# Kernel optimization log

Hardware: AMD Instinct MI355X
Metric: run time of the kernel (lower is better)

## Reference

```python
import jax, jax.numpy as jnp
import numpy as np

NUM_NETS = 100_000
PINS_PER_NET = 5
NUM_PINS = NUM_NETS * PINS_PER_NET
XL, XH, YL, YH = 0.0, 1000.0, 0.0, 1000.0
NUM_BINS_X = 512
NUM_BINS_Y = 512
BIN_SIZE_X = (XH - XL) / NUM_BINS_X
BIN_SIZE_Y = (YH - YL) / NUM_BINS_Y
NUM_H_TRACKS = 100.0
NUM_V_TRACKS = 100.0
MAX_RATE = 2.0
MIN_RATE = 1.0 / MAX_RATE


def setup_inputs() -> dict:
    key = jax.random.key(0)
    k1, k2, k3 = jax.random.split(key, 3)
    px = jax.random.uniform(k1, (NUM_PINS,), jnp.float32, XL, XH)
    py = jax.random.uniform(k2, (NUM_PINS,), jnp.float32, YL, YH)
    pin_pos = jnp.concatenate([px, py])  # [2*num_pins]: x then y
    netpin_start = (jnp.arange(NUM_NETS + 1, dtype=jnp.int32) * PINS_PER_NET)
    flat_netpin = jax.random.permutation(k3, NUM_PINS).astype(jnp.int32)
    net_weights = jnp.ones((NUM_NETS,), jnp.float32)
    return {"pin_pos": pin_pos, "netpin_start": netpin_start,
            "flat_netpin": flat_netpin, "net_weights": net_weights}


def reference(pin_pos, netpin_start, flat_netpin, net_weights):
    num_pins = flat_netpin.shape[0]
    # segment id of each flat pin slot (which net it belongs to)
    seg = jnp.searchsorted(netpin_start, jnp.arange(num_pins, dtype=netpin_start.dtype), side="right") - 1
    x = pin_pos[flat_netpin]                     # [num_pins]
    y = pin_pos[num_pins + flat_netpin]          # [num_pins]
    # per-net bounding boxes
    x_min = jax.ops.segment_min(x, seg, num_segments=NUM_NETS)
    x_max = jax.ops.segment_max(x, seg, num_segments=NUM_NETS)
    y_min = jax.ops.segment_min(y, seg, num_segments=NUM_NETS)
    y_max = jax.ops.segment_max(y, seg, num_segments=NUM_NETS)
    # fractional overlap of each net bbox with each bin column/row
    ex = XL + BIN_SIZE_X * jnp.arange(NUM_BINS_X + 1, dtype=pin_pos.dtype)
    ey = YL + BIN_SIZE_Y * jnp.arange(NUM_BINS_Y + 1, dtype=pin_pos.dtype)
    ox = jnp.maximum(jnp.minimum(x_max[:, None], ex[None, 1:]) -
                     jnp.maximum(x_min[:, None], ex[None, :-1]), 0.0)  # [N, Bx]
    oy = jnp.maximum(jnp.minimum(y_max[:, None], ey[None, 1:]) -
                     jnp.maximum(y_min[:, None], ey[None, :-1]), 0.0)  # [N, By]
    # RUDY: horizontal density wt/(y_max-y_min), vertical density wt/(x_max-x_min)
    wh = net_weights / (y_max - y_min)
    wv = net_weights / (x_max - x_min)
    h_map = jnp.einsum("nx,ny->xy", ox * wh[:, None], oy)
    v_map = jnp.einsum("nx,ny->xy", ox * wv[:, None], oy)
    h_map = h_map * (1.0 / (BIN_SIZE_X * NUM_H_TRACKS))
    v_map = v_map * (1.0 / (BIN_SIZE_Y * NUM_V_TRACKS))
    route = jnp.maximum(jnp.abs(h_map), jnp.abs(v_map))
    return jnp.clip(route * route, MIN_RATE, MAX_RATE)
```

## Files before the change

### kernel.cpp

```cpp
#include <hip/hip_runtime.h>

#define NUM_NETS     100000
#define PINS_PER_NET 5
#define NUM_PINS     (NUM_NETS * PINS_PER_NET)
#define NB           512
#define BIN_H        1.953125f
#define INV_H        0.512f
#define OUT_SCALE    (1.0f / 195.3125f)

#define SW           8
#define NSTRIPES     (NB / SW)
#define CAP          24576

#define FXS          2097152.0f
#define INV_FXS      (1.0f / 2097152.0f)

__global__ void zero_kernel(int* __restrict__ gcur) {
    gcur[threadIdx.x] = 0;
}

__global__ __launch_bounds__(256) void bbox_emit_kernel(
        const float* __restrict__ pin_pos,
        const int*   __restrict__ flat_netpin,
        const float* __restrict__ net_weights,
        int* __restrict__ gcur,
        float4* __restrict__ bucket) {
    __shared__ int lcnt[NSTRIPES];
    __shared__ int lbase[NSTRIPES];
    int tid = threadIdx.x;
    if (tid < NSTRIPES) lcnt[tid] = 0;
    __syncthreads();

    int n = blockIdx.x * 256 + tid;
    bool valid = n < NUM_NETS;
    float xmn = 1e30f, xmx = -1e30f, ymn = 1e30f, ymx = -1e30f;
    float wh = 0.f, wv = 0.f;
    int kx1 = 0, kx2 = 0;
    if (valid) {
#pragma unroll
        for (int p = 0; p < PINS_PER_NET; ++p) {
            int pi  = flat_netpin[n * PINS_PER_NET + p];
            float x = pin_pos[pi];
            float y = pin_pos[NUM_PINS + pi];
            xmn = fminf(xmn, x); xmx = fmaxf(xmx, x);
            ymn = fminf(ymn, y); ymx = fmaxf(ymx, y);
        }
        float w = net_weights[n];
        wh = w / (ymx - ymn);
        wv = w / (xmx - xmn);
        kx1 = min(NB - 1, (int)(xmn * INV_H));
        kx2 = min(NB - 1, (int)(xmx * INV_H));
#pragma unroll
        for (int cx = 0; cx < 2; ++cx) {
            int kx = cx ? kx2 : kx1;
            int s0 = kx >> 3;
            atomicAdd(&lcnt[s0], 2);
            if (kx + 1 < NB && ((kx + 1) >> 3) != s0)
                atomicAdd(&lcnt[(kx + 1) >> 3], 2);
        }
    }
    __syncthreads();
    if (tid < NSTRIPES) {
        lbase[tid] = atomicAdd(&gcur[tid], lcnt[tid]);
        lcnt[tid] = 0;
    }
    __syncthreads();
    if (valid) {
#pragma unroll
        for (int cx = 0; cx < 2; ++cx) {
            int   kx = cx ? kx2 : kx1;
            float xc = cx ? xmx : xmn;
            int s0 = kx >> 3;
            int s1 = (kx + 1 < NB) ? ((kx + 1) >> 3) : s0;
#pragma unroll
            for (int cy = 0; cy < 2; ++cy) {
                float yc = cy ? ymx : ymn;
                float sg = ((cx ^ cy) ? -1.0f : 1.0f);
                float4 item = make_float4(xc, yc, sg * wh, sg * wv);
                {
                    int rank = atomicAdd(&lcnt[s0], 1);
                    int pos  = lbase[s0] + rank;
                    if (pos < CAP) bucket[(size_t)s0 * CAP + pos] = item;
                }
                if (s1 != s0) {
                    int rank = atomicAdd(&lcnt[s1], 1);
                    int pos  = lbase[s1] + rank;
                    if (pos < CAP) bucket[(size_t)s1 * CAP + pos] = item;
                }
            }
        }
    }
}

__global__ __launch_bounds__(1024) void stripe_finish_kernel(
        const float4* __restrict__ bucket,
        const int* __restrict__ gcur,
        float* __restrict__ Th,  float* __restrict__ Tv,
        int* __restrict__ flag,
        float* __restrict__ out) {
    __shared__ int   acc[2 * SW * NB];
    __shared__ float wsc[32];
    __shared__ float offHs[2][NB];
    __shared__ float offVs[2][NB];
    int st  = blockIdx.x;
    int tid = threadIdx.x;
    int x0  = st * SW;
    int* accH = acc;
    int* accV = acc + SW * NB;
    float* fH = (float*)accH;
    float* fV = (float*)accV;

    for (int k = tid; k < 2 * SW * NB; k += 1024) acc[k] = 0;
    __syncthreads();

    int cnt = min(gcur[st], CAP);
    const float4* bk = bucket + (size_t)st * CAP;
    for (int q = tid; q < cnt; q += 1024) {
        float4 it = bk[q];
        int kx = min(NB - 1, (int)(it.x * INV_H));
        int ky = min(NB - 1, (int)(it.y * INV_H));
        float dx0 = (kx + 1) * BIN_H - it.x;
        float dx1 = it.x - kx * BIN_H;
        float dy0 = (ky + 1) * BIN_H - it.y;
        float dy1 = it.y - ky * BIN_H;
        bool y1ok = (ky + 1) < NB;
        int c = kx - x0;
#pragma unroll
        for (int cc = 0; cc < 2; ++cc) {
            int col = c + cc;
            if ((unsigned)col < SW) {
                float dx = cc ? dx1 : dx0;
                int b = col * NB + ky;
                atomicAdd(&accH[b], __float2int_rn(it.z * dx * dy0 * FXS));
                atomicAdd(&accV[b], __float2int_rn(it.w * dx * dy0 * FXS));
                if (y1ok) {
                    atomicAdd(&accH[b + 1], __float2int_rn(it.z * dx * dy1 * FXS));
                    atomicAdd(&accV[b + 1], __float2int_rn(it.w * dx * dy1 * FXS));
                }
            }
        }
    }
    __syncthreads();

    int half = tid >> 9;
    int y    = tid & 511;
    int lane = tid & 63;
    int wv16 = tid >> 6;
    int wrow0 = half * 8;
#pragma unroll
    for (int rp = 0; rp < 4; ++rp) {
        int row = rp * 2 + half;
        float vH = (float)accH[row * NB + y] * INV_FXS;
        float vV = (float)accV[row * NB + y] * INV_FXS;
#pragma unroll
        for (int o = 1; o < 64; o <<= 1) {
            float a = __shfl_up(vH, o);
            float b = __shfl_up(vV, o);
            if (lane >= o) { vH += a; vV += b; }
        }
        if (lane == 63) { wsc[wv16] = vH; wsc[16 + wv16] = vV; }
        __syncthreads();
        float oh = 0.f, ov = 0.f;
        for (int j = wrow0; j < wv16; ++j) { oh += wsc[j]; ov += wsc[16 + j]; }
        fH[row * NB + y] = vH + oh;
        fV[row * NB + y] = vV + ov;
        __syncthreads();
    }

    if (tid < NB) {
        float f = 0.f;
#pragma unroll
        for (int rr = 0; rr < SW; ++rr) {
            int i = rr * NB + tid;
            f += fH[i]; fH[i] = f;
        }
        __hip_atomic_store(&Th[st * NB + tid], f, __ATOMIC_RELAXED,
                           __HIP_MEMORY_SCOPE_AGENT);
    } else {
        int yy = tid - NB;
        float f = 0.f;
#pragma unroll
        for (int rr = 0; rr < SW; ++rr) {
            int i = rr * NB + yy;
            f += fV[i]; fV[i] = f;
        }
        __hip_atomic_store(&Tv[st * NB + yy], f, __ATOMIC_RELAXED,
                           __HIP_MEMORY_SCOPE_AGENT);
    }
    __syncthreads();
    if (tid == 0) {
        __threadfence();
        __hip_atomic_store(&flag[st], 1, __ATOMIC_RELEASE,
                           __HIP_MEMORY_SCOPE_AGENT);
    }

    if (tid < st) {
        while (__hip_atomic_load(&flag[tid], __ATOMIC_ACQUIRE,
                                 __HIP_MEMORY_SCOPE_AGENT) == 0) { }
    }
    __syncthreads();
    {
        float sh = 0.f, sv = 0.f;
        for (int s2 = half; s2 < st; s2 += 2) {
            sh += __hip_atomic_load(&Th[s2 * NB + y], __ATOMIC_RELAXED,
                                    __HIP_MEMORY_SCOPE_AGENT);
            sv += __hip_atomic_load(&Tv[s2 * NB + y], __ATOMIC_RELAXED,
                                    __HIP_MEMORY_SCOPE_AGENT);
        }
        offHs[half][y] = sh;
        offVs[half][y] = sv;
    }
    __syncthreads();

    {
        float offh = offHs[0][y] + offHs[1][y];
        float offv = offVs[0][y] + offVs[1][y];
#pragma unroll
        for (int r2 = 0; r2 < 4; ++r2) {
            int rr = half * 4 + r2;
            float h = fabsf(fH[rr * NB + y] + offh) * OUT_SCALE;
            float v = fabsf(fV[rr * NB + y] + offv) * OUT_SCALE;
            float m = fmaxf(h, v);
            out[(x0 + rr) * NB + y] = fminf(fmaxf(m * m, 0.5f), 2.0f);
        }
    }
}

__global__ void scatter_kernel(const float* __restrict__ pin_pos,
                               const int*   __restrict__ flat_netpin,
                               const float* __restrict__ net_weights,
                               float* __restrict__ Uh,
                               float* __restrict__ Uv) {
    int n = blockIdx.x * blockDim.x + threadIdx.x;
    if (n >= NUM_NETS) return;
    float xmn = 1e30f, xmx = -1e30f, ymn = 1e30f, ymx = -1e30f;
#pragma unroll
    for (int p = 0; p < PINS_PER_NET; ++p) {
        int pi  = flat_netpin[n * PINS_PER_NET + p];
        float x = pin_pos[pi];
        float y = pin_pos[NUM_PINS + pi];
        xmn = fminf(xmn, x); xmx = fmaxf(xmx, x);
        ymn = fminf(ymn, y); ymx = fmaxf(ymx, y);
    }
    float w  = net_weights[n];
    float wh = w / (ymx - ymn), wv = w / (xmx - xmn);
    int kx1 = min(NB - 1, (int)(xmn * INV_H));
    int kx2 = min(NB - 1, (int)(xmx * INV_H));
    int ky1 = min(NB - 1, (int)(ymn * INV_H));
    int ky2 = min(NB - 1, (int)(ymx * INV_H));
    int   xi[4] = { kx1, kx1 + 1, kx2, kx2 + 1 };
    float xv[4] = { (kx1 + 1) * BIN_H - xmn,  xmn - kx1 * BIN_H,
                    xmx - (kx2 + 1) * BIN_H,  kx2 * BIN_H - xmx };
    int   yi[4] = { ky1, ky1 + 1, ky2, ky2 + 1 };
    float yv[4] = { (ky1 + 1) * BIN_H - ymn,  ymn - ky1 * BIN_H,
                    ymx - (ky2 + 1) * BIN_H,  ky2 * BIN_H - ymx };
#pragma unroll
    for (int a = 0; a < 4; ++a) {
        if (xi[a] >= NB) continue;
#pragma unroll
        for (int b2 = 0; b2 < 4; ++b2) {
            if (yi[b2] >= NB) continue;
            float prod = xv[a] * yv[b2];
            atomicAdd(&Uh[xi[a] * NB + yi[b2]], wh * prod);
            atomicAdd(&Uv[xi[a] * NB + yi[b2]], wv * prod);
        }
    }
}

__global__ void fb_rowscan_kernel(float* __restrict__ Uh, float* __restrict__ Uv) {
    __shared__ float sh[NB];
    __shared__ float sv[NB];
    int rr = blockIdx.x, t = threadIdx.x;
    sh[t] = Uh[rr * NB + t];
    sv[t] = Uv[rr * NB + t];
    __syncthreads();
#pragma unroll
    for (int off = 1; off < NB; off <<= 1) {
        float a = (t >= off) ? sh[t - off] : 0.0f;
        float b = (t >= off) ? sv[t - off] : 0.0f;
        __syncthreads();
        sh[t] += a; sv[t] += b;
        __syncthreads();
    }
    Uh[rr * NB + t] = sh[t];
    Uv[rr * NB + t] = sv[t];
}

__global__ void fb_colscan_kernel(const float* __restrict__ Uh,
                                  const float* __restrict__ Uv,
                                  float* __restrict__ out) {
    int t = blockIdx.x * blockDim.x + threadIdx.x;
    if (t >= NB) return;
    float sh = 0.f, sv = 0.f;
    for (int i = 0; i < NB; ++i) {
        sh += Uh[i * NB + t];
        sv += Uv[i * NB + t];
        float h = fabsf(sh) * OUT_SCALE;
        float v = fabsf(sv) * OUT_SCALE;
        float m = fmaxf(h, v);
        out[i * NB + t] = fminf(fmaxf(m * m, 0.5f), 2.0f);
    }
}

extern "C" void kernel_launch(void* const* d_in, const int* in_sizes, int n_in,
                              void* d_out, int out_size, void* d_ws, size_t ws_size,
                              hipStream_t stream) {
    const float* pin_pos     = (const float*)d_in[0];
    const int*   flat_netpin = (const int*)d_in[2];
    const float* net_weights = (const float*)d_in[3];
    float* out = (float*)d_out;
    float* ws  = (float*)d_ws;

    const size_t o_cur = 0;
    const size_t o_flg = 64;
    const size_t o_bkt = 128;
    const size_t o_Th  = o_bkt + (size_t)NSTRIPES * CAP * 4;
    const size_t o_Tv  = o_Th + (size_t)NSTRIPES * NB;
    const size_t need  = o_Tv + (size_t)NSTRIPES * NB;

    if (ws_size < need * sizeof(float)) {
        float* Uh = ws;
        float* Uv = ws + (size_t)NB * NB;
        hipMemsetAsync(ws, 0, 2 * (size_t)NB * NB * sizeof(float), stream);
        scatter_kernel<<<(NUM_NETS + 255) / 256, 256, 0, stream>>>(
            pin_pos, flat_netpin, net_weights, Uh, Uv);
        fb_rowscan_kernel<<<NB, NB, 0, stream>>>(Uh, Uv);
        fb_colscan_kernel<<<2, 256, 0, stream>>>(Uh, Uv, out);
        return;
    }

    int*    gcur   = (int*)(ws + o_cur);
    int*    flg    = (int*)(ws + o_flg);
    float4* bucket = (float4*)(ws + o_bkt);
    float*  Th     = ws + o_Th;
    float*  Tv     = ws + o_Tv;

    zero_kernel<<<1, 128, 0, stream>>>(gcur);

    bbox_emit_kernel<<<(NUM_NETS + 255) / 256, 256, 0, stream>>>(
        pin_pos, flat_netpin, net_weights, gcur, bucket);

    stripe_finish_kernel<<<NSTRIPES, 1024, 0, stream>>>(
        bucket, gcur, Th, Tv, flg, out);
}
```

Baseline: 50.56 us.

## Fuse bbox emission and stripe finish into one persistent kernel with grid barrier

Merges the bounding-box/bucket-emit kernel and the per-stripe accumulation kernel into a single launch of 256 blocks of 1024 threads. The two phases are separated by a device-wide atomic counter barrier, and the 64 stripe blocks then continue on their own. Bucket items become pairs of relaxed 64-bit atomic stores and loads so they are visible across blocks without a kernel boundary. The global stripe-counter atomic is skipped when a block has nothing for that stripe. This removes a kernel launch gap, but all 256 blocks must be co-resident or the barrier deadlocks. Each thread now handles nets at block granularity 1024, which leaves many blocks idle in the emit phase.

```diff
diff --git a/kernel.cpp b/kernel.cpp
--- a/kernel.cpp
+++ b/kernel.cpp
@@ -11,27 +11,37 @@
 #define SW           8
 #define NSTRIPES     (NB / SW)
 #define CAP          24576
+#define GBLK         256
 
 #define FXS          2097152.0f
 #define INV_FXS      (1.0f / 2097152.0f)
 
-__global__ void zero_kernel(int* __restrict__ gcur) {
-    gcur[threadIdx.x] = 0;
-}
-
-__global__ __launch_bounds__(256) void bbox_emit_kernel(
+__global__ void zero_kernel(int* __restrict__ p) {
+    if (threadIdx.x < 160) p[threadIdx.x] = 0;
+}
+
+__global__ __launch_bounds__(1024) void fused_kernel(
         const float* __restrict__ pin_pos,
         const int*   __restrict__ flat_netpin,
         const float* __restrict__ net_weights,
         int* __restrict__ gcur,
-        float4* __restrict__ bucket) {
-    __shared__ int lcnt[NSTRIPES];
-    __shared__ int lbase[NSTRIPES];
+        unsigned long long* __restrict__ bkt64,
+        float* __restrict__ Th,  float* __restrict__ Tv,
+        int* __restrict__ flag, int* __restrict__ done,
+        float* __restrict__ out) {
+    __shared__ int   lcnt[NSTRIPES];
+    __shared__ int   lbase[NSTRIPES];
+    __shared__ int   acc[2 * SW * NB];
+    __shared__ float wsc[32];
+    __shared__ float offHs[2][NB];
+    __shared__ float offVs[2][NB];
     int tid = threadIdx.x;
+    int bid = blockIdx.x;
+
     if (tid < NSTRIPES) lcnt[tid] = 0;
     __syncthreads();
 
-    int n = blockIdx.x * 256 + tid;
+    int n = bid * 1024 + tid;
     bool valid = n < NUM_NETS;
     float xmn = 1e30f, xmx = -1e30f, ymn = 1e30f, ymx = -1e30f;
     float wh = 0.f, wv = 0.f;
@@ -61,7 +71,8 @@
     }
     __syncthreads();
     if (tid < NSTRIPES) {
-        lbase[tid] = atomicAdd(&gcur[tid], lcnt[tid]);
+        int c = lcnt[tid];
+        lbase[tid] = c ? atomicAdd(&gcur[tid], c) : 0;
         lcnt[tid] = 0;
     }
     __syncthreads();
@@ -76,35 +87,52 @@
             for (int cy = 0; cy < 2; ++cy) {
                 float yc = cy ? ymx : ymn;
                 float sg = ((cx ^ cy) ? -1.0f : 1.0f);
-                float4 item = make_float4(xc, yc, sg * wh, sg * wv);
+                unsigned long long lo =
+                    (unsigned long long)__float_as_uint(xc) |
+                    ((unsigned long long)__float_as_uint(yc) << 32);
+                unsigned long long hi =
+                    (unsigned long long)__float_as_uint(sg * wh) |
+                    ((unsigned long long)__float_as_uint(sg * wv) << 32);
                 {
                     int rank = atomicAdd(&lcnt[s0], 1);
                     int pos  = lbase[s0] + rank;
-                    if (pos < CAP) bucket[(size_t)s0 * CAP + pos] = item;
+                    if (pos < CAP) {
+                        size_t ip = ((size_t)s0 * CAP + pos) * 2;
+                        __hip_atomic_store(&bkt64[ip], lo, __ATOMIC_RELAXED,
+                                           __HIP_MEMORY_SCOPE_AGENT);
+                        __hip_atomic_store(&bkt64[ip + 1], hi, __ATOMIC_RELAXED,
+                                           __HIP_MEMORY_SCOPE_AGENT);
+                    }
                 }
                 if (s1 != s0) {
                     int rank = atomicAdd(&lcnt[s1], 1);
                     int pos  = lbase[s1] + rank;
-                    if (pos < CAP) bucket[(size_t)s1 * CAP + pos] = item;
+                    if (pos < CAP) {
+                        size_t ip = ((size_t)s1 * CAP + pos) * 2;
+                        __hip_atomic_store(&bkt64[ip], lo, __ATOMIC_RELAXED,
+                                           __HIP_MEMORY_SCOPE_AGENT);
+                        __hip_atomic_store(&bkt64[ip + 1], hi, __ATOMIC_RELAXED,
+                                           __HIP_MEMORY_SCOPE_AGENT);
+                    }
                 }
             }
         }
     }
-}
-
-__global__ __launch_bounds__(1024) void stripe_finish_kernel(
-        const float4* __restrict__ bucket,
-        const int* __restrict__ gcur,
-        float* __restrict__ Th,  float* __restrict__ Tv,
-        int* __restrict__ flag,
-        float* __restrict__ out) {
-    __shared__ int   acc[2 * SW * NB];
-    __shared__ float wsc[32];
-    __shared__ float offHs[2][NB];
-    __shared__ float offVs[2][NB];
-    int st  = blockIdx.x;
-    int tid = threadIdx.x;
-    int x0  = st * SW;
+    __syncthreads();
+
+    if (tid == 0) {
+        atomicAdd(done, 1);
+        while (__hip_atomic_load(done, __ATOMIC_ACQUIRE,
+                                 __HIP_MEMORY_SCOPE_AGENT) < GBLK) {
+            __builtin_amdgcn_s_sleep(4);
+        }
+    }
+    __syncthreads();
+
+    if (bid >= NSTRIPES) return;
+
+    int st = bid;
+    int x0 = st * SW;
     int* accH = acc;
     int* accV = acc + SW * NB;
     float* fH = (float*)accH;
@@ -113,16 +141,24 @@
     for (int k = tid; k < 2 * SW * NB; k += 1024) acc[k] = 0;
     __syncthreads();
 
-    int cnt = min(gcur[st], CAP);
-    const float4* bk = bucket + (size_t)st * CAP;
+    int cnt = min(__hip_atomic_load(&gcur[st], __ATOMIC_RELAXED,
+                                    __HIP_MEMORY_SCOPE_AGENT), CAP);
     for (int q = tid; q < cnt; q += 1024) {
-        float4 it = bk[q];
-        int kx = min(NB - 1, (int)(it.x * INV_H));
-        int ky = min(NB - 1, (int)(it.y * INV_H));
-        float dx0 = (kx + 1) * BIN_H - it.x;
-        float dx1 = it.x - kx * BIN_H;
-        float dy0 = (ky + 1) * BIN_H - it.y;
-        float dy1 = it.y - ky * BIN_H;
+        size_t ip = ((size_t)st * CAP + q) * 2;
+        unsigned long long lo = __hip_atomic_load(&bkt64[ip], __ATOMIC_RELAXED,
+                                                  __HIP_MEMORY_SCOPE_AGENT);
+        unsigned long long hi = __hip_atomic_load(&bkt64[ip + 1], __ATOMIC_RELAXED,
+                                                  __HIP_MEMORY_SCOPE_AGENT);
+        float ix = __uint_as_float((unsigned)lo);
+        float iy = __uint_as_float((unsigned)(lo >> 32));
+        float iz = __uint_as_float((unsigned)hi);
+        float iw = __uint_as_float((unsigned)(hi >> 32));
+        int kx = min(NB - 1, (int)(ix * INV_H));
+        int ky = min(NB - 1, (int)(iy * INV_H));
+        float dx0 = (kx + 1) * BIN_H - ix;
+        float dx1 = ix - kx * BIN_H;
+        float dy0 = (ky + 1) * BIN_H - iy;
+        float dy1 = iy - ky * BIN_H;
         bool y1ok = (ky + 1) < NB;
         int c = kx - x0;
 #pragma unroll
@@ -131,11 +167,11 @@
             if ((unsigned)col < SW) {
                 float dx = cc ? dx1 : dx0;
                 int b = col * NB + ky;
-                atomicAdd(&accH[b], __float2int_rn(it.z * dx * dy0 * FXS));
-                atomicAdd(&accV[b], __float2int_rn(it.w * dx * dy0 * FXS));
+                atomicAdd(&accH[b], __float2int_rn(iz * dx * dy0 * FXS));
+                atomicAdd(&accV[b], __float2int_rn(iw * dx * dy0 * FXS));
                 if (y1ok) {
-                    atomicAdd(&accH[b + 1], __float2int_rn(it.z * dx * dy1 * FXS));
-                    atomicAdd(&accV[b + 1], __float2int_rn(it.w * dx * dy1 * FXS));
+                    atomicAdd(&accH[b + 1], __float2int_rn(iz * dx * dy1 * FXS));
+                    atomicAdd(&accV[b + 1], __float2int_rn(iw * dx * dy1 * FXS));
                 }
             }
         }
@@ -196,7 +232,9 @@
 
     if (tid < st) {
         while (__hip_atomic_load(&flag[tid], __ATOMIC_ACQUIRE,
-                                 __HIP_MEMORY_SCOPE_AGENT) == 0) { }
+                                 __HIP_MEMORY_SCOPE_AGENT) == 0) {
+            __builtin_amdgcn_s_sleep(2);
+        }
     }
     __syncthreads();
     {
@@ -311,12 +349,13 @@
     float* out = (float*)d_out;
     float* ws  = (float*)d_ws;
 
-    const size_t o_cur = 0;
-    const size_t o_flg = 64;
-    const size_t o_bkt = 128;
-    const size_t o_Th  = o_bkt + (size_t)NSTRIPES * CAP * 4;
-    const size_t o_Tv  = o_Th + (size_t)NSTRIPES * NB;
-    const size_t need  = o_Tv + (size_t)NSTRIPES * NB;
+    const size_t o_cur  = 0;
+    const size_t o_flg  = 64;
+    const size_t o_done = 128;
+    const size_t o_bkt  = 160;
+    const size_t o_Th   = o_bkt + (size_t)NSTRIPES * CAP * 4;
+    const size_t o_Tv   = o_Th + (size_t)NSTRIPES * NB;
+    const size_t need   = o_Tv + (size_t)NSTRIPES * NB;
 
     if (ws_size < need * sizeof(float)) {
         float* Uh = ws;
@@ -329,17 +368,15 @@
         return;
     }
 
-    int*    gcur   = (int*)(ws + o_cur);
-    int*    flg    = (int*)(ws + o_flg);
-    float4* bucket = (float4*)(ws + o_bkt);
-    float*  Th     = ws + o_Th;
-    float*  Tv     = ws + o_Tv;
-
-    zero_kernel<<<1, 128, 0, stream>>>(gcur);
-
-    bbox_emit_kernel<<<(NUM_NETS + 255) / 256, 256, 0, stream>>>(
-        pin_pos, flat_netpin, net_weights, gcur, bucket);
-
-    stripe_finish_kernel<<<NSTRIPES, 1024, 0, stream>>>(
-        bucket, gcur, Th, Tv, flg, out);
-}
+    int*                gcur  = (int*)(ws + o_cur);
+    int*                flg   = (int*)(ws + o_flg);
+    int*                done  = (int*)(ws + o_done);
+    unsigned long long* bkt64 = (unsigned long long*)(ws + o_bkt);
+    float*              Th    = ws + o_Th;
+    float*              Tv    = ws + o_Tv;
+
+    zero_kernel<<<1, 256, 0, stream>>>((int*)ws);
+
+    fused_kernel<<<GBLK, 1024, 0, stream>>>(
+        pin_pos, flat_netpin, net_weights, gcur, bkt64, Th, Tv, flg, done, out);
+}
```

Result: slower. 157.6 us (+211.7%).

## Split each x-stripe into two y-half blocks with cross-block row-total exchange

Applied to the files above, without the earlier changes.

Buckets are now keyed by stripe and y-half, so the finish stage launches twice as many blocks, each owning an 8x256 tile instead of 8x512. Items whose cell straddles the y=255/256 boundary are emitted to both halves. The upper-half block waits on a flag for the lower half's per-row totals to complete its y prefix scan, and the cross-stripe lookback now runs per half. The aim is more CU parallelism and less shared-memory atomic and scan work per block. The cost is extra emitted items, an additional inter-block spin dependency, and reliance on all blocks being co-resident.

```diff
diff --git a/kernel.cpp b/kernel.cpp
--- a/kernel.cpp
+++ b/kernel.cpp
@@ -10,13 +10,15 @@
 
 #define SW           8
 #define NSTRIPES     (NB / SW)
-#define CAP          24576
+#define NBK          (NSTRIPES * 2)
+#define HH           256
+#define CAP          12288
 
 #define FXS          2097152.0f
 #define INV_FXS      (1.0f / 2097152.0f)
 
-__global__ void zero_kernel(int* __restrict__ gcur) {
-    gcur[threadIdx.x] = 0;
+__global__ void zero_kernel(int* __restrict__ p) {
+    if (threadIdx.x < 320) p[threadIdx.x] = 0;
 }
 
 __global__ __launch_bounds__(256) void bbox_emit_kernel(
@@ -25,17 +27,17 @@
         const float* __restrict__ net_weights,
         int* __restrict__ gcur,
         float4* __restrict__ bucket) {
-    __shared__ int lcnt[NSTRIPES];
-    __shared__ int lbase[NSTRIPES];
+    __shared__ int lcnt[NBK];
+    __shared__ int lbase[NBK];
     int tid = threadIdx.x;
-    if (tid < NSTRIPES) lcnt[tid] = 0;
+    if (tid < NBK) lcnt[tid] = 0;
     __syncthreads();
 
     int n = blockIdx.x * 256 + tid;
     bool valid = n < NUM_NETS;
     float xmn = 1e30f, xmx = -1e30f, ymn = 1e30f, ymx = -1e30f;
     float wh = 0.f, wv = 0.f;
-    int kx1 = 0, kx2 = 0;
+    int kx1 = 0, kx2 = 0, ky1 = 0, ky2 = 0;
     if (valid) {
 #pragma unroll
         for (int p = 0; p < PINS_PER_NET; ++p) {
@@ -50,18 +52,31 @@
         wv = w / (xmx - xmn);
         kx1 = min(NB - 1, (int)(xmn * INV_H));
         kx2 = min(NB - 1, (int)(xmx * INV_H));
+        ky1 = min(NB - 1, (int)(ymn * INV_H));
+        ky2 = min(NB - 1, (int)(ymx * INV_H));
 #pragma unroll
         for (int cx = 0; cx < 2; ++cx) {
             int kx = cx ? kx2 : kx1;
             int s0 = kx >> 3;
-            atomicAdd(&lcnt[s0], 2);
-            if (kx + 1 < NB && ((kx + 1) >> 3) != s0)
-                atomicAdd(&lcnt[(kx + 1) >> 3], 2);
-        }
-    }
-    __syncthreads();
-    if (tid < NSTRIPES) {
-        lbase[tid] = atomicAdd(&gcur[tid], lcnt[tid]);
+            int s1 = (kx + 1 < NB && ((kx + 1) >> 3) != s0) ? ((kx + 1) >> 3) : -1;
+#pragma unroll
+            for (int cy = 0; cy < 2; ++cy) {
+                int ky = cy ? ky2 : ky1;
+                int hh = ky >> 8;
+                bool ystr = (ky == 255);
+                atomicAdd(&lcnt[(s0 << 1) | hh], 1);
+                if (ystr)     atomicAdd(&lcnt[(s0 << 1) | 1], 1);
+                if (s1 >= 0) {
+                    atomicAdd(&lcnt[(s1 << 1) | hh], 1);
+                    if (ystr) atomicAdd(&lcnt[(s1 << 1) | 1], 1);
+                }
+            }
+        }
+    }
+    __syncthreads();
+    if (tid < NBK) {
+        int c = lcnt[tid];
+        lbase[tid] = c ? atomicAdd(&gcur[tid], c) : 0;
         lcnt[tid] = 0;
     }
     __syncthreads();
@@ -71,157 +86,211 @@
             int   kx = cx ? kx2 : kx1;
             float xc = cx ? xmx : xmn;
             int s0 = kx >> 3;
-            int s1 = (kx + 1 < NB) ? ((kx + 1) >> 3) : s0;
+            int s1 = (kx + 1 < NB && ((kx + 1) >> 3) != s0) ? ((kx + 1) >> 3) : -1;
 #pragma unroll
             for (int cy = 0; cy < 2; ++cy) {
+                int   ky = cy ? ky2 : ky1;
                 float yc = cy ? ymx : ymn;
+                int hh = ky >> 8;
+                bool ystr = (ky == 255);
                 float sg = ((cx ^ cy) ? -1.0f : 1.0f);
                 float4 item = make_float4(xc, yc, sg * wh, sg * wv);
-                {
-                    int rank = atomicAdd(&lcnt[s0], 1);
-                    int pos  = lbase[s0] + rank;
-                    if (pos < CAP) bucket[(size_t)s0 * CAP + pos] = item;
+                int bs[4]; int nb = 0;
+                bs[nb++] = (s0 << 1) | hh;
+                if (ystr)     bs[nb++] = (s0 << 1) | 1;
+                if (s1 >= 0) {
+                    bs[nb++] = (s1 << 1) | hh;
+                    if (ystr) bs[nb++] = (s1 << 1) | 1;
                 }
-                if (s1 != s0) {
-                    int rank = atomicAdd(&lcnt[s1], 1);
-                    int pos  = lbase[s1] + rank;
-                    if (pos < CAP) bucket[(size_t)s1 * CAP + pos] = item;
+                for (int j = 0; j < nb; ++j) {
+                    int b = bs[j];
+                    int rank = atomicAdd(&lcnt[b], 1);
+                    int pos  = lbase[b] + rank;
+                    if (pos < CAP) bucket[(size_t)b * CAP + pos] = item;
                 }
             }
         }
     }
 }
 
-__global__ __launch_bounds__(1024) void stripe_finish_kernel(
+__global__ __launch_bounds__(1024) void half_stripe_kernel(
         const float4* __restrict__ bucket,
         const int* __restrict__ gcur,
+        float* __restrict__ rtH, float* __restrict__ rtV,
+        int* __restrict__ flagRT,
         float* __restrict__ Th,  float* __restrict__ Tv,
-        int* __restrict__ flag,
+        int* __restrict__ flagT,
         float* __restrict__ out) {
-    __shared__ int   acc[2 * SW * NB];
-    __shared__ float wsc[32];
-    __shared__ float offHs[2][NB];
-    __shared__ float offVs[2][NB];
-    int st  = blockIdx.x;
+    __shared__ int   acc[2 * SW * HH];
+    __shared__ float wsc[4][4][2];
+    __shared__ float rowtH[8], rowtV[8];
+    __shared__ float btH[8],  btV[8];
+    __shared__ float offH[4][HH];
+    __shared__ float offV[4][HH];
+    int bid = blockIdx.x;
+    int st  = bid >> 1;
+    int h   = bid & 1;
     int tid = threadIdx.x;
     int x0  = st * SW;
+    int y0  = h * HH;
     int* accH = acc;
-    int* accV = acc + SW * NB;
+    int* accV = acc + SW * HH;
     float* fH = (float*)accH;
     float* fV = (float*)accV;
 
-    for (int k = tid; k < 2 * SW * NB; k += 1024) acc[k] = 0;
-    __syncthreads();
-
-    int cnt = min(gcur[st], CAP);
-    const float4* bk = bucket + (size_t)st * CAP;
+    for (int k = tid; k < 2 * SW * HH; k += 1024) acc[k] = 0;
+    __syncthreads();
+
+    int cnt = min(gcur[bid], CAP);
+    const float4* bk = bucket + (size_t)bid * CAP;
     for (int q = tid; q < cnt; q += 1024) {
         float4 it = bk[q];
         int kx = min(NB - 1, (int)(it.x * INV_H));
         int ky = min(NB - 1, (int)(it.y * INV_H));
+        int gy = ky - y0;
         float dx0 = (kx + 1) * BIN_H - it.x;
         float dx1 = it.x - kx * BIN_H;
         float dy0 = (ky + 1) * BIN_H - it.y;
         float dy1 = it.y - ky * BIN_H;
-        bool y1ok = (ky + 1) < NB;
+        bool ok0 = (unsigned)gy < (unsigned)HH;
+        bool ok1 = (ky + 1 < NB) && ((unsigned)(gy + 1) < (unsigned)HH);
         int c = kx - x0;
 #pragma unroll
         for (int cc = 0; cc < 2; ++cc) {
             int col = c + cc;
             if ((unsigned)col < SW) {
                 float dx = cc ? dx1 : dx0;
-                int b = col * NB + ky;
-                atomicAdd(&accH[b], __float2int_rn(it.z * dx * dy0 * FXS));
-                atomicAdd(&accV[b], __float2int_rn(it.w * dx * dy0 * FXS));
-                if (y1ok) {
-                    atomicAdd(&accH[b + 1], __float2int_rn(it.z * dx * dy1 * FXS));
-                    atomicAdd(&accV[b + 1], __float2int_rn(it.w * dx * dy1 * FXS));
+                if (ok0) {
+                    int b = col * HH + gy;
+                    atomicAdd(&accH[b], __float2int_rn(it.z * dx * dy0 * FXS));
+                    atomicAdd(&accV[b], __float2int_rn(it.w * dx * dy0 * FXS));
+                }
+                if (ok1) {
+                    int b = col * HH + gy + 1;
+                    atomicAdd(&accH[b], __float2int_rn(it.z * dx * dy1 * FXS));
+                    atomicAdd(&accV[b], __float2int_rn(it.w * dx * dy1 * FXS));
                 }
             }
         }
     }
     __syncthreads();
 
-    int half = tid >> 9;
-    int y    = tid & 511;
     int lane = tid & 63;
-    int wv16 = tid >> 6;
-    int wrow0 = half * 8;
-#pragma unroll
-    for (int rp = 0; rp < 4; ++rp) {
-        int row = rp * 2 + half;
-        float vH = (float)accH[row * NB + y] * INV_FXS;
-        float vV = (float)accV[row * NB + y] * INV_FXS;
+    int wwi  = (tid >> 6) & 3;
+    int rg   = tid >> 8;
+    int y    = tid & 255;
+#pragma unroll
+    for (int pass = 0; pass < 2; ++pass) {
+        int row = pass * 4 + rg;
+        float vH = (float)accH[row * HH + y] * INV_FXS;
+        float vV = (float)accV[row * HH + y] * INV_FXS;
 #pragma unroll
         for (int o = 1; o < 64; o <<= 1) {
             float a = __shfl_up(vH, o);
             float b = __shfl_up(vV, o);
             if (lane >= o) { vH += a; vV += b; }
         }
-        if (lane == 63) { wsc[wv16] = vH; wsc[16 + wv16] = vV; }
+        if (lane == 63) { wsc[rg][wwi][0] = vH; wsc[rg][wwi][1] = vV; }
         __syncthreads();
         float oh = 0.f, ov = 0.f;
-        for (int j = wrow0; j < wv16; ++j) { oh += wsc[j]; ov += wsc[16 + j]; }
-        fH[row * NB + y] = vH + oh;
-        fV[row * NB + y] = vV + ov;
-        __syncthreads();
-    }
-
-    if (tid < NB) {
+        for (int j = 0; j < wwi; ++j) { oh += wsc[rg][j][0]; ov += wsc[rg][j][1]; }
+        vH += oh; vV += ov;
+        fH[row * HH + y] = vH;
+        fV[row * HH + y] = vV;
+        if (lane == 63 && wwi == 3) { rowtH[row] = vH; rowtV[row] = vV; }
+        __syncthreads();
+    }
+
+    if (h == 0) {
+        if (tid < 8) {
+            __hip_atomic_store(&rtH[st * 8 + tid], rowtH[tid], __ATOMIC_RELAXED,
+                               __HIP_MEMORY_SCOPE_AGENT);
+            __hip_atomic_store(&rtV[st * 8 + tid], rowtV[tid], __ATOMIC_RELAXED,
+                               __HIP_MEMORY_SCOPE_AGENT);
+        }
+        if (tid < 8) { btH[tid] = 0.f; btV[tid] = 0.f; }
+        __syncthreads();
+        if (tid == 0) {
+            __threadfence();
+            __hip_atomic_store(&flagRT[st], 1, __ATOMIC_RELEASE,
+                               __HIP_MEMORY_SCOPE_AGENT);
+        }
+    } else {
+        if (tid == 0) {
+            while (__hip_atomic_load(&flagRT[st], __ATOMIC_ACQUIRE,
+                                     __HIP_MEMORY_SCOPE_AGENT) == 0) {
+                __builtin_amdgcn_s_sleep(2);
+            }
+        }
+        __syncthreads();
+        if (tid < 8) {
+            btH[tid] = __hip_atomic_load(&rtH[st * 8 + tid], __ATOMIC_RELAXED,
+                                         __HIP_MEMORY_SCOPE_AGENT);
+            btV[tid] = __hip_atomic_load(&rtV[st * 8 + tid], __ATOMIC_RELAXED,
+                                         __HIP_MEMORY_SCOPE_AGENT);
+        }
+        __syncthreads();
+    }
+
+    if (tid < HH) {
         float f = 0.f;
 #pragma unroll
         for (int rr = 0; rr < SW; ++rr) {
-            int i = rr * NB + tid;
-            f += fH[i]; fH[i] = f;
-        }
-        __hip_atomic_store(&Th[st * NB + tid], f, __ATOMIC_RELAXED,
+            int i = rr * HH + tid;
+            f += fH[i] + btH[rr];
+            fH[i] = f;
+        }
+        __hip_atomic_store(&Th[bid * HH + tid], f, __ATOMIC_RELAXED,
                            __HIP_MEMORY_SCOPE_AGENT);
-    } else {
-        int yy = tid - NB;
+    } else if (tid < 2 * HH) {
+        int yy = tid - HH;
         float f = 0.f;
 #pragma unroll
         for (int rr = 0; rr < SW; ++rr) {
-            int i = rr * NB + yy;
-            f += fV[i]; fV[i] = f;
-        }
-        __hip_atomic_store(&Tv[st * NB + yy], f, __ATOMIC_RELAXED,
+            int i = rr * HH + yy;
+            f += fV[i] + btV[rr];
+            fV[i] = f;
+        }
+        __hip_atomic_store(&Tv[bid * HH + yy], f, __ATOMIC_RELAXED,
                            __HIP_MEMORY_SCOPE_AGENT);
     }
     __syncthreads();
     if (tid == 0) {
         __threadfence();
-        __hip_atomic_store(&flag[st], 1, __ATOMIC_RELEASE,
+        __hip_atomic_store(&flagT[bid], 1, __ATOMIC_RELEASE,
                            __HIP_MEMORY_SCOPE_AGENT);
     }
 
     if (tid < st) {
-        while (__hip_atomic_load(&flag[tid], __ATOMIC_ACQUIRE,
-                                 __HIP_MEMORY_SCOPE_AGENT) == 0) { }
+        while (__hip_atomic_load(&flagT[tid * 2 + h], __ATOMIC_ACQUIRE,
+                                 __HIP_MEMORY_SCOPE_AGENT) == 0) {
+            __builtin_amdgcn_s_sleep(2);
+        }
     }
     __syncthreads();
     {
         float sh = 0.f, sv = 0.f;
-        for (int s2 = half; s2 < st; s2 += 2) {
-            sh += __hip_atomic_load(&Th[s2 * NB + y], __ATOMIC_RELAXED,
+        for (int s2 = rg; s2 < st; s2 += 4) {
+            sh += __hip_atomic_load(&Th[(s2 * 2 + h) * HH + y], __ATOMIC_RELAXED,
                                     __HIP_MEMORY_SCOPE_AGENT);
-            sv += __hip_atomic_load(&Tv[s2 * NB + y], __ATOMIC_RELAXED,
+            sv += __hip_atomic_load(&Tv[(s2 * 2 + h) * HH + y], __ATOMIC_RELAXED,
                                     __HIP_MEMORY_SCOPE_AGENT);
         }
-        offHs[half][y] = sh;
-        offVs[half][y] = sv;
+        offH[rg][y] = sh;
+        offV[rg][y] = sv;
     }
     __syncthreads();
 
     {
-        float offh = offHs[0][y] + offHs[1][y];
-        float offv = offVs[0][y] + offVs[1][y];
-#pragma unroll
-        for (int r2 = 0; r2 < 4; ++r2) {
-            int rr = half * 4 + r2;
-            float h = fabsf(fH[rr * NB + y] + offh) * OUT_SCALE;
-            float v = fabsf(fV[rr * NB + y] + offv) * OUT_SCALE;
-            float m = fmaxf(h, v);
-            out[(x0 + rr) * NB + y] = fminf(fmaxf(m * m, 0.5f), 2.0f);
+        float oh = offH[0][y] + offH[1][y] + offH[2][y] + offH[3][y];
+        float ov = offV[0][y] + offV[1][y] + offV[2][y] + offV[3][y];
+#pragma unroll
+        for (int r2 = 0; r2 < 2; ++r2) {
+            int rr = rg * 2 + r2;
+            float hv = fabsf(fH[rr * HH + y] + oh) * OUT_SCALE;
+            float vv = fabsf(fV[rr * HH + y] + ov) * OUT_SCALE;
+            float m = fmaxf(hv, vv);
+            out[(x0 + rr) * NB + y0 + y] = fminf(fmaxf(m * m, 0.5f), 2.0f);
         }
     }
 }
@@ -312,11 +381,14 @@
     float* ws  = (float*)d_ws;
 
     const size_t o_cur = 0;
-    const size_t o_flg = 64;
-    const size_t o_bkt = 128;
-    const size_t o_Th  = o_bkt + (size_t)NSTRIPES * CAP * 4;
-    const size_t o_Tv  = o_Th + (size_t)NSTRIPES * NB;
-    const size_t need  = o_Tv + (size_t)NSTRIPES * NB;
+    const size_t o_fRT = 128;
+    const size_t o_fT  = 192;
+    const size_t o_rtH = 320;
+    const size_t o_rtV = o_rtH + 512;
+    const size_t o_bkt = o_rtV + 512;
+    const size_t o_Th  = o_bkt + (size_t)NBK * CAP * 4;
+    const size_t o_Tv  = o_Th + (size_t)NBK * HH;
+    const size_t need  = o_Tv + (size_t)NBK * HH;
 
     if (ws_size < need * sizeof(float)) {
         float* Uh = ws;
@@ -330,16 +402,19 @@
     }
 
     int*    gcur   = (int*)(ws + o_cur);
-    int*    flg    = (int*)(ws + o_flg);
+    int*    fRT    = (int*)(ws + o_fRT);
+    int*    fT     = (int*)(ws + o_fT);
+    float*  rtH    = ws + o_rtH;
+    float*  rtV    = ws + o_rtV;
     float4* bucket = (float4*)(ws + o_bkt);
     float*  Th     = ws + o_Th;
     float*  Tv     = ws + o_Tv;
 
-    zero_kernel<<<1, 128, 0, stream>>>(gcur);
+    zero_kernel<<<1, 512, 0, stream>>>((int*)ws);
 
     bbox_emit_kernel<<<(NUM_NETS + 255) / 256, 256, 0, stream>>>(
         pin_pos, flat_netpin, net_weights, gcur, bucket);
 
-    stripe_finish_kernel<<<NSTRIPES, 1024, 0, stream>>>(
-        bucket, gcur, Th, Tv, flg, out);
-}
+    half_stripe_kernel<<<NBK, 1024, 0, stream>>>(
+        bucket, gcur, rtH, rtV, fRT, Th, Tv, fT, out);
+}
```

Result: no change. 51.34 us (+1.5%).
